# Kernel tuning notes

Measured on AMD Instinct MI355X. Metric: run time of the kernel, lower is better.

Reference implementation:

```python
import jax, jax.numpy as jnp
import numpy as np

# MxCorrelation (MXNet/FlowNet correlation) parameters
PAD = 4            # pad_size
K = 1              # kernel_size
MAXD = 4           # max_displacement
S1 = 1             # stride1 (output stride)
S2 = 1             # stride2 (displacement stride)


def setup_inputs() -> dict:
    key = jax.random.key(0)
    k1, k2 = jax.random.split(key)
    B, C, H, W = 8, 128, 128, 128
    input1 = jax.random.normal(k1, (B, C, H, W), dtype=jnp.float32)
    input2 = jax.random.normal(k2, (B, C, H, W), dtype=jnp.float32)
    return {"input1": input1, "input2": input2}


def _correlation(a, b):
    # a, b: [B, C, H, W]; returns [B, gw*gw, top_h, top_w]
    B, C, H, W = a.shape
    kr = (K - 1) // 2                       # kernel radius
    border = MAXD + kr                      # border in padded coords
    pa = jnp.pad(a, ((0, 0), (0, 0), (PAD, PAD), (PAD, PAD)))
    pb = jnp.pad(b, ((0, 0), (0, 0), (PAD, PAD), (PAD, PAD)))
    Hp, Wp = H + 2 * PAD, W + 2 * PAD
    th = -(-(Hp - 2 * border) // S1)        # top_height (ceil div)
    tw = -(-(Wp - 2 * border) // S1)        # top_width
    ngr = MAXD // S2                        # neighborhood grid radius
    gw = 2 * ngr + 1                        # grid width -> gw*gw out channels
    sumelems = jnp.float32(K * K * C)       # MXNet normalization

    out = []
    # channel order matches MXNet: row displacement p outer, col q inner
    for p in range(-ngr, ngr + 1):
        for q in range(-ngr, ngr + 1):
            s2p, s2q = p * S2, q * S2
            acc = jnp.zeros((B, th, tw), dtype=a.dtype)
            for dy in range(-kr, kr + 1):
                for dx in range(-kr, kr + 1):
                    A = pa[:, :, border + dy: border + dy + th * S1: S1,
                           border + dx: border + dx + tw * S1: S1]
                    Bm = pb[:, :, border + s2p + dy: border + s2p + dy + th * S1: S1,
                            border + s2q + dx: border + s2q + dx + tw * S1: S1]
                    acc = acc + jnp.sum(A * Bm, axis=1)  # reduce over channels
            out.append(acc / sumelems)
    return jnp.stack(out, axis=1)  # [B, gw*gw, th, tw]


def reference(input1, input2):
    return _correlation(input1, input2)
```

## Files before the change

kernel.cpp:

```cpp
#include <hip/hip_runtime.h>


typedef __fp16 h2 __attribute__((ext_vector_type(2)));

#define BW2 144

#if __has_builtin(__builtin_amdgcn_fdot2)
  #define FDOT2(a, b, c) __builtin_amdgcn_fdot2((a), (b), (c), false)
#else
  static __device__ inline float FDOT2(h2 a, h2 b, float c) {
      return c + (float)a.x * (float)b.x + (float)a.y * (float)b.y;
  }
#endif

static __device__ inline float pk2f(float lo, float hi) {
    h2 v = __builtin_amdgcn_cvt_pkrtz(lo, hi);
    return __builtin_bit_cast(float, v);
}
static __device__ inline h2 f2h2(float f) { return __builtin_bit_cast(h2, f); }

__global__ __launch_bounds__(192, 4)
void corr_kernel(const float* __restrict__ A, const float* __restrict__ B,
                 float* __restrict__ out)
{
    const int bidx = blockIdx.x;
    const int bb = bidx & 7;
    const int t2 = bidx >> 3;
    const int y  = t2 & 127;
    const int pg = t2 >> 7;

    const int tid  = threadIdx.x;
    const int wave = tid >> 6;
    const int lane = tid & 63;
    const int cs   = lane >> 5;
    const int x0   = (lane & 31) << 2;
    const int pr   = pg * 3 + wave;

    __shared__ h2 a_s[2][2][128];
    __shared__ h2 b_s[2][3][2][BW2];

    {
        float4* p = (float4*)&a_s[0][0][0];
        const int na = 2 * 2 * 128 / 4;
        for (int i = tid; i < na; i += 192) p[i] = make_float4(0.f, 0.f, 0.f, 0.f);
        float4* pb = (float4*)&b_s[0][0][0][0];
        const int nb = 2 * 3 * 2 * BW2 / 4;
        for (int i = tid; i < nb; i += 192) pb[i] = make_float4(0.f, 0.f, 0.f, 0.f);
    }

    float acc[9][4];
    #pragma unroll
    for (int q = 0; q < 9; ++q)
        #pragma unroll
        for (int i = 0; i < 4; ++i) acc[q][i] = 0.f;

    const long plane = 128L * 128L;
    const float* Abase = A + (long)bb * 128 * plane + (long)y * 128;
    const float* Bbase = B + (long)bb * 128 * plane;

    const int i4  = (tid & 31) << 2;
    const int rp  = tid >> 5;
    const int brw = rp >> 1;
    const int bpp = rp & 1;
    const int bys = y + pg * 3 + brw - 4;
    const bool bval = (unsigned)bys < 128u;
    const float* Bsrc = Bbase + (long)bys * 128 + i4;

    const bool aact = tid < 64;
    const int app = (tid >> 5) & 1;

    float4 rb0 = make_float4(0.f,0.f,0.f,0.f), rb1 = rb0, ra0 = rb0, ra1 = rb0;

    auto load_chunk = [&](int ch0) {
        if (bval) {
            const int c0 = ch0 + (bpp << 1);
            rb0 = *(const float4*)(Bsrc + (long)c0 * plane);
            rb1 = *(const float4*)(Bsrc + (long)(c0 + 1) * plane);
        }
        if (aact) {
            const int c0 = ch0 + (app << 1);
            ra0 = *(const float4*)(Abase + (long)c0 * plane + i4);
            ra1 = *(const float4*)(Abase + (long)(c0 + 1) * plane + i4);
        }
    };
    auto write_stage = [&](int buf) {
        if (bval) {
            float4 w;
            w.x = pk2f(rb0.x, rb1.x);
            w.y = pk2f(rb0.y, rb1.y);
            w.z = pk2f(rb0.z, rb1.z);
            w.w = pk2f(rb0.w, rb1.w);
            *(float4*)&b_s[buf][brw][bpp][4 + i4] = w;
        }
        if (aact) {
            float4 w;
            w.x = pk2f(ra0.x, ra1.x);
            w.y = pk2f(ra0.y, ra1.y);
            w.z = pk2f(ra0.z, ra1.z);
            w.w = pk2f(ra0.w, ra1.w);
            *(float4*)&a_s[buf][app][i4] = w;
        }
    };

    load_chunk(0);
    __syncthreads();
    write_stage(0);
    load_chunk(4);
    __syncthreads();

    for (int k = 0; k < 32; ++k) {
        const int buf = k & 1;
        if (k + 1 < 32) write_stage(buf ^ 1);
        if (k + 2 < 32) load_chunk((k + 2) << 2);
        {
            const float4 av = *(const float4*)&a_s[buf][cs][x0];
            const float4 b0 = *(const float4*)&b_s[buf][wave][cs][x0];
            const float4 b1 = *(const float4*)&b_s[buf][wave][cs][x0 + 4];
            const float4 b2 = *(const float4*)&b_s[buf][wave][cs][x0 + 8];
            const h2 a2[4] = { f2h2(av.x), f2h2(av.y), f2h2(av.z), f2h2(av.w) };
            const h2 w[12] = { f2h2(b0.x), f2h2(b0.y), f2h2(b0.z), f2h2(b0.w),
                               f2h2(b1.x), f2h2(b1.y), f2h2(b1.z), f2h2(b1.w),
                               f2h2(b2.x), f2h2(b2.y), f2h2(b2.z), f2h2(b2.w) };
            #pragma unroll
            for (int q = 0; q < 9; ++q)
                #pragma unroll
                for (int i = 0; i < 4; ++i)
                    acc[q][i] = FDOT2(a2[i], w[q + i], acc[q][i]);
        }
        __syncthreads();
    }

    #pragma unroll
    for (int q = 0; q < 9; ++q)
        #pragma unroll
        for (int i = 0; i < 4; ++i)
            acc[q][i] += __shfl_down(acc[q][i], 32);

    if (cs == 0) {
        const float scale = 1.0f / 128.0f;
        float* obase = out + (((long)bb * 81 + (long)pr * 9) * 128 + y) * 128 + x0;
        #pragma unroll
        for (int q = 0; q < 9; ++q) {
            const float4 v = make_float4(acc[q][0] * scale, acc[q][1] * scale,
                                         acc[q][2] * scale, acc[q][3] * scale);
            *(float4*)(obase + (long)q * plane) = v;
        }
    }
}

extern "C" void kernel_launch(void* const* d_in, const int* in_sizes, int n_in,
                              void* d_out, int out_size, void* d_ws, size_t ws_size,
                              hipStream_t stream) {
    const float* a = (const float*)d_in[0];
    const float* b = (const float*)d_in[1];
    float* out = (float*)d_out;
    hipLaunchKernelGGL(corr_kernel, dim3(3072), dim3(192), 0, stream, a, b, out);
}
```

Baseline: 199.5 us.

## Deepen register prefetch to two chunks and use LDS-only barriers

Register prefetch now runs three chunks ahead with two register sets instead of one, so more global-load latency is hidden. The main loop is unrolled by two so buffer indices are compile-time constants. The LDS writes for the next stage move after the compute. __syncthreads is replaced by a barrier that waits only on LDS counters, which lets outstanding global loads stay in flight across barriers. This costs extra registers, which may reduce occupancy under the launch bounds.

```diff
diff --git a/kernel.cpp b/kernel.cpp
--- a/kernel.cpp
+++ b/kernel.cpp
@@ -19,6 +19,13 @@
 }
 static __device__ inline h2 f2h2(float f) { return __builtin_bit_cast(h2, f); }
 
+#define BARRIER() do {                                    \
+    asm volatile("" ::: "memory");                        \
+    asm volatile("s_waitcnt lgkmcnt(0)" ::: "memory");    \
+    __builtin_amdgcn_s_barrier();                         \
+    asm volatile("" ::: "memory");                        \
+} while (0)
+
 __global__ __launch_bounds__(192, 4)
 void corr_kernel(const float* __restrict__ A, const float* __restrict__ B,
                  float* __restrict__ out)
@@ -38,15 +45,6 @@
 
     __shared__ h2 a_s[2][2][128];
     __shared__ h2 b_s[2][3][2][BW2];
-
-    {
-        float4* p = (float4*)&a_s[0][0][0];
-        const int na = 2 * 2 * 128 / 4;
-        for (int i = tid; i < na; i += 192) p[i] = make_float4(0.f, 0.f, 0.f, 0.f);
-        float4* pb = (float4*)&b_s[0][0][0][0];
-        const int nb = 2 * 3 * 2 * BW2 / 4;
-        for (int i = tid; i < nb; i += 192) pb[i] = make_float4(0.f, 0.f, 0.f, 0.f);
-    }
 
     float acc[9][4];
     #pragma unroll
@@ -69,66 +67,86 @@
     const bool aact = tid < 64;
     const int app = (tid >> 5) & 1;
 
-    float4 rb0 = make_float4(0.f,0.f,0.f,0.f), rb1 = rb0, ra0 = rb0, ra1 = rb0;
+    float4 rb0[2], rb1[2], ra0[2], ra1[2];
 
-    auto load_chunk = [&](int ch0) {
-        if (bval) {
-            const int c0 = ch0 + (bpp << 1);
-            rb0 = *(const float4*)(Bsrc + (long)c0 * plane);
-            rb1 = *(const float4*)(Bsrc + (long)(c0 + 1) * plane);
-        }
-        if (aact) {
-            const int c0 = ch0 + (app << 1);
-            ra0 = *(const float4*)(Abase + (long)c0 * plane + i4);
-            ra1 = *(const float4*)(Abase + (long)(c0 + 1) * plane + i4);
-        }
-    };
-    auto write_stage = [&](int buf) {
-        if (bval) {
-            float4 w;
-            w.x = pk2f(rb0.x, rb1.x);
-            w.y = pk2f(rb0.y, rb1.y);
-            w.z = pk2f(rb0.z, rb1.z);
-            w.w = pk2f(rb0.w, rb1.w);
-            *(float4*)&b_s[buf][brw][bpp][4 + i4] = w;
-        }
-        if (aact) {
-            float4 w;
-            w.x = pk2f(ra0.x, ra1.x);
-            w.y = pk2f(ra0.y, ra1.y);
-            w.z = pk2f(ra0.z, ra1.z);
-            w.w = pk2f(ra0.w, ra1.w);
-            *(float4*)&a_s[buf][app][i4] = w;
-        }
-    };
+#define LOADC(CHUNK, S) do {                                             \
+    const int ch0_ = (CHUNK) << 2;                                       \
+    if (bval) {                                                          \
+        const int c0_ = ch0_ + (bpp << 1);                               \
+        rb0[(S)] = *(const float4*)(Bsrc + (long)c0_ * plane);           \
+        rb1[(S)] = *(const float4*)(Bsrc + (long)(c0_ + 1) * plane);     \
+    }                                                                    \
+    if (aact) {                                                          \
+        const int c0_ = ch0_ + (app << 1);                               \
+        ra0[(S)] = *(const float4*)(Abase + (long)c0_ * plane + i4);     \
+        ra1[(S)] = *(const float4*)(Abase + (long)(c0_ + 1) * plane + i4);\
+    }                                                                    \
+} while (0)
 
-    load_chunk(0);
-    __syncthreads();
-    write_stage(0);
-    load_chunk(4);
-    __syncthreads();
+#define STAGE(S) do {                                                    \
+    if (bval) {                                                          \
+        float4 w_;                                                       \
+        w_.x = pk2f(rb0[(S)].x, rb1[(S)].x);                             \
+        w_.y = pk2f(rb0[(S)].y, rb1[(S)].y);                             \
+        w_.z = pk2f(rb0[(S)].z, rb1[(S)].z);                             \
+        w_.w = pk2f(rb0[(S)].w, rb1[(S)].w);                             \
+        *(float4*)&b_s[(S)][brw][bpp][4 + i4] = w_;       \
+    }                                                                    \
+    if (aact) {                                                          \
+        float4 w_;                                                       \
+        w_.x = pk2f(ra0[(S)].x, ra1[(S)].x);                             \
+        w_.y = pk2f(ra0[(S)].y, ra1[(S)].y);                             \
+        w_.z = pk2f(ra0[(S)].z, ra1[(S)].z);                             \
+        w_.w = pk2f(ra0[(S)].w, ra1[(S)].w);                             \
+        *(float4*)&a_s[(S)][app][i4] = w_;                               \
+    }                                                                    \
+} while (0)
 
-    for (int k = 0; k < 32; ++k) {
-        const int buf = k & 1;
-        if (k + 1 < 32) write_stage(buf ^ 1);
-        if (k + 2 < 32) load_chunk((k + 2) << 2);
-        {
-            const float4 av = *(const float4*)&a_s[buf][cs][x0];
-            const float4 b0 = *(const float4*)&b_s[buf][wave][cs][x0];
-            const float4 b1 = *(const float4*)&b_s[buf][wave][cs][x0 + 4];
-            const float4 b2 = *(const float4*)&b_s[buf][wave][cs][x0 + 8];
-            const h2 a2[4] = { f2h2(av.x), f2h2(av.y), f2h2(av.z), f2h2(av.w) };
-            const h2 w[12] = { f2h2(b0.x), f2h2(b0.y), f2h2(b0.z), f2h2(b0.w),
-                               f2h2(b1.x), f2h2(b1.y), f2h2(b1.z), f2h2(b1.w),
-                               f2h2(b2.x), f2h2(b2.y), f2h2(b2.z), f2h2(b2.w) };
-            #pragma unroll
-            for (int q = 0; q < 9; ++q)
-                #pragma unroll
-                for (int i = 0; i < 4; ++i)
-                    acc[q][i] = FDOT2(a2[i], w[q + i], acc[q][i]);
-        }
-        __syncthreads();
+#define BODY(K, S) do {                                                          \
+    {                                                                            \
+        const float4 av  = *(const float4*)&a_s[(S)][cs][x0];                    \
+        const float4 b0v = *(const float4*)&b_s[(S)][wave][cs][x0];              \
+        const float4 b1v = *(const float4*)&b_s[(S)][wave][cs][x0 + 4];          \
+        const float4 b2v = *(const float4*)&b_s[(S)][wave][cs][x0 + 8];          \
+        const h2 a2[4] = { f2h2(av.x), f2h2(av.y), f2h2(av.z), f2h2(av.w) };     \
+        const h2 w[12] = { f2h2(b0v.x), f2h2(b0v.y), f2h2(b0v.z), f2h2(b0v.w),   \
+                           f2h2(b1v.x), f2h2(b1v.y), f2h2(b1v.z), f2h2(b1v.w),   \
+                           f2h2(b2v.x), f2h2(b2v.y), f2h2(b2v.z), f2h2(b2v.w) }; \
+        _Pragma("unroll")                                                        \
+        for (int q = 0; q < 9; ++q)                                              \
+            _Pragma("unroll")                                                    \
+            for (int i = 0; i < 4; ++i)                                          \
+                acc[q][i] = FDOT2(a2[i], w[q + i], acc[q][i]);                   \
+    }                                                                            \
+    if ((K) + 1 < 32) STAGE((S) ^ 1);                                            \
+    if ((K) + 3 < 32) LOADC((K) + 3, (S) ^ 1);                                   \
+    BARRIER();                                                                   \
+} while (0)
+
+    LOADC(0, 0);
+    LOADC(1, 1);
+
+    {
+        float4* pa = (float4*)&a_s[0][0][0];
+        const int na = 2 * 2 * 128 / 4;
+        for (int i = tid; i < na; i += 192) pa[i] = make_float4(0.f, 0.f, 0.f, 0.f);
+        float4* pb = (float4*)&b_s[0][0][0][0];
+        const int nb = 2 * 3 * 2 * BW2 / 4;
+        for (int i = tid; i < nb; i += 192) pb[i] = make_float4(0.f, 0.f, 0.f, 0.f);
     }
+    BARRIER();
+    STAGE(0);
+    LOADC(2, 0);
+    BARRIER();
+
+    for (int k = 0; k < 32; k += 2) {
+        BODY(k, 0);
+        BODY(k + 1, 1);
+    }
+
+#undef BODY
+#undef STAGE
+#undef LOADC
 
     #pragma unroll
     for (int q = 0; q < 9; ++q)
```

Measured after the change: 212.9 us. +6.7%, slower.
